# Performance work log

Hardware: AMD Instinct MI355X
Metric: run time of the kernel (lower is better)

## Reference

```python
import jax, jax.numpy as jnp
import numpy as np

B, S, D = 4, 2048, 512
H, DQK, DV = 6, 64, 64
PROJ = (DQK + DQK + DV) * H  # 1152
EPS = 1e-5


def setup_inputs() -> dict:
    key = jax.random.key(0)
    ks = jax.random.split(key, 5)
    sc = 0.05
    return {
        "x": jax.random.normal(ks[0], (B, S, D), jnp.float32),
        "Wp": jax.random.normal(ks[1], (PROJ, D), jnp.float32) * sc,
        "bp": jax.random.normal(ks[2], (PROJ,), jnp.float32) * sc,
        "Wo": jax.random.normal(ks[3], (D, H * DV), jnp.float32) * sc,
        "bo": jax.random.normal(ks[4], (D,), jnp.float32) * sc,
        "gamma": jnp.ones((D,), jnp.float32),
        "beta": jnp.zeros((D,), jnp.float32),
    }


def reference(x, Wp, bp, Wo, bo, gamma, beta):
    b, s, d = x.shape
    # 1x1 Conv1d projection == pointwise linear: [b,s,d] @ [d,proj] -> [b,s,proj]
    proj = jnp.einsum("bsd,pd->bsp", x, Wp) + bp
    q, k, v = proj[..., : H * DQK], proj[..., H * DQK : 2 * H * DQK], proj[..., 2 * H * DQK :]
    # split heads -> [b,h,s,depth]
    q = q.reshape(b, s, H, DQK).transpose(0, 2, 1, 3)
    k = k.reshape(b, s, H, DQK).transpose(0, 2, 1, 3)
    v = v.reshape(b, s, H, DV).transpose(0, 2, 1, 3)
    scores = jnp.einsum("bhqd,bhkd->bhqk", q, k) / jnp.sqrt(jnp.float32(DQK))
    attn = jax.nn.softmax(scores, axis=-1)  # softmax over kv axis
    out = jnp.einsum("bhqk,bhkd->bhqd", attn, v)
    # concat heads -> [b,s,h*dv]
    concat = out.transpose(0, 2, 1, 3).reshape(b, s, H * DV)
    y = jnp.einsum("bsf,df->bsd", concat, Wo) + bo
    z = x + y
    mu = jnp.mean(z, axis=-1, keepdims=True)
    var = jnp.mean(jnp.square(z - mu), axis=-1, keepdims=True)
    return (z - mu) / jnp.sqrt(var + EPS) * gamma + beta
```

## Files before the change

kernel.cpp:

```cpp
#include <hip/hip_runtime.h>

typedef __bf16 bf16;
typedef __bf16 bf16x8 __attribute__((ext_vector_type(8)));
typedef __bf16 bf16x4 __attribute__((ext_vector_type(4)));
typedef float  f32x4  __attribute__((ext_vector_type(4)));

#define BB 4
#define SS 2048
#define DD 512
#define HH 6
#define DH 64
#define PROJ 1152
#define FF 384
#define LDK 72

__device__ __forceinline__ bool probe_fp32(const unsigned* p) {
    return p[0] == 0x3F800000u;
}

__device__ __forceinline__ float fast_exp2(float x) {
#if __has_builtin(__builtin_amdgcn_exp2f)
    return __builtin_amdgcn_exp2f(x);
#else
    return __expf(x * 0.69314718f);
#endif
}

struct CvtSrcs { const void* s[7]; };

#define CB0 524288
#define CB1 598016
#define CB2 622592
#define CB3 622736
#define CB4 622800
#define CB5 622864
#define CB6 622928

__global__ __launch_bounds__(256) void cvt_all_kernel(
    CvtSrcs srcs, bf16* __restrict__ dst, const unsigned* __restrict__ probe)
{
    const int t = blockIdx.x * 256 + threadIdx.x;
    if (t >= CB6) return;
    int seg, base;
    if      (t < CB0) { seg = 0; base = 0;   }
    else if (t < CB1) { seg = 1; base = CB0; }
    else if (t < CB2) { seg = 2; base = CB1; }
    else if (t < CB3) { seg = 3; base = CB2; }
    else if (t < CB4) { seg = 4; base = CB3; }
    else if (t < CB5) { seg = 5; base = CB4; }
    else              { seg = 6; base = CB5; }
    const int li = (t - base) * 8;
    if (probe_fp32(probe)) {
        const float* s = (const float*)srcs.s[seg] + li;
        bf16x8 o;
#pragma unroll
        for (int j = 0; j < 8; ++j) o[j] = (bf16)s[j];
        *(bf16x8*)&dst[(size_t)t * 8] = o;
    } else {
        *(bf16x8*)&dst[(size_t)t * 8] =
            *(const bf16x8*)((const bf16*)srcs.s[seg] + li);
    }
}

template<int MERGE>
__global__ __launch_bounds__(256) void gemm_bt_kernel(
    const bf16* __restrict__ A, const float* __restrict__ lpart,
    const bf16* __restrict__ B, const bf16* __restrict__ bias,
    bf16* __restrict__ Cout, int M, int N, int K)
{
    __shared__ __attribute__((aligned(16))) bf16 sA[64 * LDK];
    __shared__ __attribute__((aligned(16))) bf16 sB[128 * LDK];

    const int tid  = threadIdx.x;
    const int lane = tid & 63;
    const int wave = tid >> 6;
    const int wn = wave * 32;
    const int l15 = lane & 15;
    const int quad = lane >> 4;
    const int bm = blockIdx.x * 64;
    const int bn = blockIdx.y * 128;
    const int KT = K / 64;

    int srowA[2], srowB[4];
    const int scol = (tid & 7) << 3;
#pragma unroll
    for (int j = 0; j < 2; ++j) srowA[j] = (j * 256 + tid) >> 3;
#pragma unroll
    for (int j = 0; j < 4; ++j) srowB[j] = (j * 256 + tid) >> 3;

    const bf16* pA[2]; const bf16* pB[4];
    const float* pl0[2];
#pragma unroll
    for (int j = 0; j < 2; ++j) {
        if (MERGE) {
            int row = bm + srowA[j];
            int b = row >> 11, q = row & (SS - 1);
            pA[j]  = A + ((size_t)(b * HH) * SS + q) * DH + scol;
            pl0[j] = lpart + (size_t)(b * HH) * SS + q;
        } else {
            pA[j] = A + (size_t)(bm + srowA[j]) * K + scol;
        }
    }
#pragma unroll
    for (int j = 0; j < 4; ++j)
        pB[j] = B + (size_t)(bn + srowB[j]) * K + scol;

    bf16x8 arb[2], a1b[2], brb[4];
    float l0[2], l1[2];

    auto loadAB = [&]() {
#pragma unroll
        for (int j = 0; j < 2; ++j) {
            arb[j] = *(const bf16x8*)pA[j];
            if (MERGE) {
                a1b[j] = *(const bf16x8*)(pA[j] + (size_t)BB * HH * SS * DH);
                l0[j] = pl0[j][0];
                l1[j] = pl0[j][(size_t)BB * HH * SS];
                pA[j]  += (size_t)SS * DH;
                pl0[j] += SS;
            } else {
                pA[j] += 64;
            }
        }
#pragma unroll
        for (int j = 0; j < 4; ++j) {
            brb[j] = *(const bf16x8*)pB[j];
            pB[j] += 64;
        }
    };

    loadAB();

    const f32x4 fzero = {0.f, 0.f, 0.f, 0.f};
    f32x4 acc[4][2];
#pragma unroll
    for (int mi = 0; mi < 4; ++mi)
#pragma unroll
        for (int ni = 0; ni < 2; ++ni) acc[mi][ni] = fzero;

    for (int kt = 0; kt < KT; ++kt) {
        __syncthreads();
#pragma unroll
        for (int j = 0; j < 2; ++j) {
            if (MERGE) {
                float inv = 1.f / (l0[j] + l1[j]);
                bf16x8 m;
#pragma unroll
                for (int e = 0; e < 8; ++e)
                    m[e] = (bf16)(((float)arb[j][e] + (float)a1b[j][e]) * inv);
                *(bf16x8*)&sA[srowA[j] * LDK + scol] = m;
            } else {
                *(bf16x8*)&sA[srowA[j] * LDK + scol] = arb[j];
            }
        }
#pragma unroll
        for (int j = 0; j < 4; ++j)
            *(bf16x8*)&sB[srowB[j] * LDK + scol] = brb[j];
        __syncthreads();
        if (kt + 1 < KT) loadAB();

#pragma unroll
        for (int kk = 0; kk < 2; ++kk) {
            bf16x8 af[4], bfr[2];
#pragma unroll
            for (int i = 0; i < 4; ++i)
                af[i] = *(const bf16x8*)&sA[(i * 16 + l15) * LDK + kk * 32 + quad * 8];
#pragma unroll
            for (int i = 0; i < 2; ++i)
                bfr[i] = *(const bf16x8*)&sB[(wn + i * 16 + l15) * LDK + kk * 32 + quad * 8];
#pragma unroll
            for (int mi = 0; mi < 4; ++mi)
#pragma unroll
                for (int ni = 0; ni < 2; ++ni)
                    acc[mi][ni] = __builtin_amdgcn_mfma_f32_16x16x32_bf16(
                        af[mi], bfr[ni], acc[mi][ni], 0, 0, 0);
        }
    }

#pragma unroll
    for (int mi = 0; mi < 4; ++mi) {
        int row = bm + mi * 16 + quad * 4;
#pragma unroll
        for (int ni = 0; ni < 2; ++ni) {
            int col = bn + wn + ni * 16 + l15;
            float bv = (float)bias[col];
#pragma unroll
            for (int r = 0; r < 4; ++r)
                Cout[(size_t)(row + r) * N + col] = (bf16)(acc[mi][ni][r] + bv);
        }
    }
}

__global__ __launch_bounds__(256) void vt_kernel(
    const bf16* __restrict__ proj, bf16* __restrict__ Vt)
{
    __shared__ __attribute__((aligned(16))) bf16 lt[64 * LDK];

    const int tid = threadIdx.x;
    const int s0 = blockIdx.x * 64;
    const int bh = blockIdx.y;
    const int b = bh / HH, h = bh % HH;

#pragma unroll
    for (int i = 0; i < 2; ++i) {
        int vid = i * 256 + tid;
        int sl = vid >> 3;
        int dc = (vid & 7) << 3;
        bf16x8 v = *(const bf16x8*)&proj[
            (size_t)(b * SS + s0 + sl) * PROJ + 2 * HH * DH + h * DH + dc];
#pragma unroll
        for (int j = 0; j < 8; ++j) {
            int d = dc + j;
            lt[d * LDK + (sl ^ (((d >> 3) & 3) * 8))] = v[j];
        }
    }
    __syncthreads();

#pragma unroll
    for (int i = 0; i < 2; ++i) {
        int vid = i * 256 + tid;
        int d = vid >> 3;
        int sc = (vid & 7) << 3;
        bf16x8 v = *(const bf16x8*)&lt[d * LDK + (sc ^ (((d >> 3) & 3) * 8))];
        *(bf16x8*)&Vt[(size_t)bh * DH * SS + (size_t)d * SS + s0 + sc] = v;
    }
}

__global__ __launch_bounds__(256) void attn_kernel(
    const bf16* __restrict__ proj, const bf16* __restrict__ Vt,
    bf16* __restrict__ Opart, float* __restrict__ lpart)
{
    __shared__ __attribute__((aligned(16))) bf16 sK [2][64 * 64];
    __shared__ __attribute__((aligned(16))) bf16 sVt[2][64 * 64];
    __shared__ __attribute__((aligned(16))) bf16 sP [4 * 32 * 64];

    const int tid  = threadIdx.x;
    const int lane = tid & 63;
    const int wave = tid >> 6;
    const int l15  = lane & 15;
    const int quad = lane >> 4;

    const int bh = blockIdx.y;
    const int b = bh / HH, h = bh % HH;
    const int q0 = blockIdx.x * 128;
    const int kz = blockIdx.z;
    const bf16* base = proj + (size_t)b * SS * PROJ;
    const bf16* vtb  = Vt + (size_t)bh * DH * SS;

    const int sr = tid >> 3;
    const int sc = (tid & 7) << 3;

    const float QS = 0.18033688f;
    bf16x8 qf[2][2];
#pragma unroll
    for (int g = 0; g < 2; ++g) {
        const int qrow = q0 + wave * 32 + g * 16 + l15;
#pragma unroll
        for (int ks = 0; ks < 2; ++ks) {
            qf[ks][g] = *(const bf16x8*)&base[
                (size_t)qrow * PROJ + h * DH + ks * 32 + quad * 8];
#pragma unroll
            for (int j = 0; j < 8; ++j)
                qf[ks][g][j] = (bf16)((float)qf[ks][g][j] * QS);
        }
    }

    const f32x4 fzero = {0.f, 0.f, 0.f, 0.f};
    f32x4 lacc[2] = {fzero, fzero};
    f32x4 oacc[2][4];
#pragma unroll
    for (int g = 0; g < 2; ++g)
#pragma unroll
        for (int fi = 0; fi < 4; ++fi) oacc[g][fi] = fzero;

    bf16* pw = &sP[wave * 32 * 64];

    const int kt0 = kz * (SS / 128);
    const int kt1 = kt0 + SS / 128;

    const bf16* pk[2]; const bf16* pv[2];
#pragma unroll
    for (int i = 0; i < 2; ++i) {
        int r = i * 32 + sr;
        pk[i] = &base[(size_t)(kt0 * 64 + r) * PROJ + HH * DH + h * DH + sc];
        pv[i] = &vtb[(size_t)r * SS + kt0 * 64 + sc];
    }

    bf16x8 kr[2], vr[2];
    auto loadKV = [&]() {
#pragma unroll
        for (int i = 0; i < 2; ++i) {
            kr[i] = *(const bf16x8*)pk[i];
            vr[i] = *(const bf16x8*)pv[i];
            pk[i] += (size_t)64 * PROJ;
            pv[i] += 64;
        }
    };
    auto stage = [&](int buf) {
#pragma unroll
        for (int i = 0; i < 2; ++i) {
            int r = i * 32 + sr;
            const int swc = sc ^ ((r & 7) << 3);
            *(bf16x8*)&sK [buf][r * 64 + swc] = kr[i];
            *(bf16x8*)&sVt[buf][r * 64 + swc] = vr[i];
        }
    };

    loadKV();
    stage(0);
    loadKV();

    for (int t = kt0; t < kt1; ++t) {
        const int cur = t & 1;
        __syncthreads();
        if (t + 1 < kt1) {
            stage(cur ^ 1);
            if (t + 2 < kt1) loadKV();
        }

        f32x4 st[2][4];
#pragma unroll
        for (int mi = 0; mi < 4; ++mi) {
            const int row = mi * 16 + l15;
            const int sw = (row & 7) << 3;
            bf16x8 af0 = *(const bf16x8*)&sK[cur][row * 64 + ((quad * 8) ^ sw)];
            bf16x8 af1 = *(const bf16x8*)&sK[cur][row * 64 + ((32 + quad * 8) ^ sw)];
            __builtin_amdgcn_s_setprio(1);
#pragma unroll
            for (int g = 0; g < 2; ++g) {
                st[g][mi] = __builtin_amdgcn_mfma_f32_16x16x32_bf16(
                    af0, qf[0][g], fzero, 0, 0, 0);
                st[g][mi] = __builtin_amdgcn_mfma_f32_16x16x32_bf16(
                    af1, qf[1][g], st[g][mi], 0, 0, 0);
            }
            __builtin_amdgcn_s_setprio(0);
        }

#pragma unroll
        for (int g = 0; g < 2; ++g)
#pragma unroll
            for (int mi = 0; mi < 4; ++mi) {
#pragma unroll
                for (int r = 0; r < 4; ++r)
                    st[g][mi][r] = fast_exp2(st[g][mi][r]);
                lacc[g] += st[g][mi];
            }

#pragma unroll
        for (int g = 0; g < 2; ++g) {
            const int r = g * 16 + l15;
            const int sw = (r & 7) << 3;
#pragma unroll
            for (int mi = 0; mi < 4; ++mi) {
                bf16x4 p4;
#pragma unroll
                for (int e = 0; e < 4; ++e) p4[e] = (bf16)st[g][mi][e];
                *(bf16x4*)&pw[r * 64 + ((mi * 16 + quad * 4) ^ sw)] = p4;
            }
        }

#pragma unroll
        for (int ks = 0; ks < 2; ++ks) {
            bf16x8 bfrag[2];
#pragma unroll
            for (int g = 0; g < 2; ++g) {
                const int r = g * 16 + l15;
                bfrag[g] = *(const bf16x8*)&pw[
                    r * 64 + ((ks * 32 + quad * 8) ^ ((r & 7) << 3))];
            }
#pragma unroll
            for (int fi = 0; fi < 4; ++fi) {
                const int row = fi * 16 + l15;
                bf16x8 af = *(const bf16x8*)&sVt[cur][
                    row * 64 + ((ks * 32 + quad * 8) ^ ((row & 7) << 3))];
                __builtin_amdgcn_s_setprio(1);
#pragma unroll
                for (int g = 0; g < 2; ++g)
                    oacc[g][fi] = __builtin_amdgcn_mfma_f32_16x16x32_bf16(
                        af, bfrag[g], oacc[g][fi], 0, 0, 0);
                __builtin_amdgcn_s_setprio(0);
            }
        }
    }

    float l_part[2];
#pragma unroll
    for (int g = 0; g < 2; ++g) {
        l_part[g] = lacc[g][0] + lacc[g][1] + lacc[g][2] + lacc[g][3];
        l_part[g] += __shfl_xor(l_part[g], 16);
        l_part[g] += __shfl_xor(l_part[g], 32);
    }

    const size_t zoff = (size_t)(kz * BB * HH + bh) * SS;
#pragma unroll
    for (int g = 0; g < 2; ++g) {
        const int qg = q0 + wave * 32 + g * 16 + l15;
        bf16* orow = Opart + (zoff + qg) * DH;
#pragma unroll
        for (int fi = 0; fi < 4; ++fi) {
            bf16x4 o4;
#pragma unroll
            for (int r = 0; r < 4; ++r) o4[r] = (bf16)oacc[g][fi][r];
            *(bf16x4*)&orow[fi * 16 + quad * 4] = o4;
        }
    }
    if (lane < 16) {
#pragma unroll
        for (int g = 0; g < 2; ++g)
            lpart[zoff + q0 + wave * 32 + g * 16 + lane] = l_part[g];
    }
}

__global__ __launch_bounds__(256) void ln_kernel(
    const bf16* __restrict__ x, const bf16* __restrict__ y,
    const bf16* __restrict__ gamma, const bf16* __restrict__ beta,
    void* __restrict__ out, const unsigned* __restrict__ probe)
{
    const bool f32 = probe_fp32(probe);
    const int lane = threadIdx.x & 63;
    const int wave = threadIdx.x >> 6;
    const int row = blockIdx.x * 4 + wave;
    const size_t off = (size_t)row * DD + lane * 8;

    bf16x8 xv = *(const bf16x8*)&x[off];
    bf16x8 yv = *(const bf16x8*)&y[off];
    float z[8];
    float s = 0.f;
#pragma unroll
    for (int j = 0; j < 8; ++j) { z[j] = (float)xv[j] + (float)yv[j]; s += z[j]; }
#pragma unroll
    for (int m = 1; m < 64; m <<= 1) s += __shfl_xor(s, m);
    float mu = s * (1.f / DD);
    float s2 = 0.f;
#pragma unroll
    for (int j = 0; j < 8; ++j) { float d = z[j] - mu; s2 += d * d; }
#pragma unroll
    for (int m = 1; m < 64; m <<= 1) s2 += __shfl_xor(s2, m);
    float rs = rsqrtf(s2 * (1.f / DD) + 1e-5f);

    bf16x8 gm = *(const bf16x8*)&gamma[lane * 8];
    bf16x8 be = *(const bf16x8*)&beta[lane * 8];
    if (f32) {
        f32x4 o0, o1;
#pragma unroll
        for (int j = 0; j < 4; ++j) {
            o0[j] = (z[j]     - mu) * rs * (float)gm[j]     + (float)be[j];
            o1[j] = (z[j + 4] - mu) * rs * (float)gm[j + 4] + (float)be[j + 4];
        }
        *(f32x4*)&((float*)out)[off]     = o0;
        *(f32x4*)&((float*)out)[off + 4] = o1;
    } else {
        bf16x8 o;
#pragma unroll
        for (int j = 0; j < 8; ++j)
            o[j] = (bf16)((z[j] - mu) * rs * (float)gm[j] + (float)be[j]);
        *(bf16x8*)&((bf16*)out)[off] = o;
    }
}

extern "C" void kernel_launch(void* const* d_in, const int* in_sizes, int n_in,
                              void* d_out, int out_size, void* d_ws, size_t ws_size,
                              hipStream_t stream)
{
    const unsigned* probe = (const unsigned*)d_in[5];

    char* ws = (char*)d_ws;
    size_t o = 0;
    bf16* xb   = (bf16*)(ws + o); o += (size_t)BB * SS * DD * 2;
    bf16* Wpb  = (bf16*)(ws + o); o += (size_t)PROJ * DD * 2;
    bf16* Wob  = (bf16*)(ws + o); o += (size_t)DD * FF * 2;
    bf16* bpb  = (bf16*)(ws + o); o += PROJ * 2;
    bf16* bob  = (bf16*)(ws + o); o += DD * 2;
    bf16* gb   = (bf16*)(ws + o); o += DD * 2;
    bf16* bb   = (bf16*)(ws + o); o += DD * 2;
    bf16* proj   = (bf16*)(ws + o); o += (size_t)BB * SS * PROJ * 2;
    bf16* vtbuf  = (bf16*)(ws + o); o += (size_t)BB * HH * DH * SS * 2;
    bf16* Opart  = (bf16*)(ws + o); o += (size_t)2 * BB * HH * SS * DH * 2;
    float* lpart = (float*)(ws + o); o += (size_t)2 * BB * HH * SS * 4;
    bf16* ybuf = proj;

    CvtSrcs srcs;
    srcs.s[0] = d_in[0]; srcs.s[1] = d_in[1]; srcs.s[2] = d_in[3];
    srcs.s[3] = d_in[2]; srcs.s[4] = d_in[4]; srcs.s[5] = d_in[5];
    srcs.s[6] = d_in[6];
    cvt_all_kernel<<<(CB6 + 255) / 256, 256, 0, stream>>>(srcs, xb, probe);

    gemm_bt_kernel<0><<<dim3((BB * SS) / 64, PROJ / 128), 256, 0, stream>>>(
        xb, nullptr, Wpb, bpb, proj, BB * SS, PROJ, DD);
    vt_kernel<<<dim3(SS / 64, BB * HH), 256, 0, stream>>>(proj, vtbuf);
    attn_kernel<<<dim3(SS / 128, BB * HH, 2), 256, 0, stream>>>(
        proj, vtbuf, Opart, lpart);
    gemm_bt_kernel<1><<<dim3((BB * SS) / 64, DD / 128), 256, 0, stream>>>(
        Opart, lpart, Wob, bob, ybuf, BB * SS, DD, FF);
    ln_kernel<<<dim3((BB * SS) / 4), 256, 0, stream>>>(
        xb, ybuf, gb, bb, d_out, probe);
}
```

Before: 155.7 us.

## Load K/V MFMA fragments directly from global memory, dropping shared staging

The attention kernel no longer stages K and V^T tiles through double-buffered shared memory with block-wide barriers. Each wave now loads its own MFMA fragments for K and V straight from global memory into registers, prefetching the next tile between the QK and PV phases. This removes the __syncthreads and LDS traffic, but all four waves redundantly fetch the same K/V data (4x more global/L2 traffic), uses more registers, and performs strided uncoalesced row loads.

```diff
diff --git a/kernel.cpp b/kernel.cpp
--- a/kernel.cpp
+++ b/kernel.cpp
@@ -230,9 +230,7 @@
     const bf16* __restrict__ proj, const bf16* __restrict__ Vt,
     bf16* __restrict__ Opart, float* __restrict__ lpart)
 {
-    __shared__ __attribute__((aligned(16))) bf16 sK [2][64 * 64];
-    __shared__ __attribute__((aligned(16))) bf16 sVt[2][64 * 64];
-    __shared__ __attribute__((aligned(16))) bf16 sP [4 * 32 * 64];
+    __shared__ __attribute__((aligned(16))) bf16 sP[4 * 32 * 64];
 
     const int tid  = threadIdx.x;
     const int lane = tid & 63;
@@ -245,10 +243,8 @@
     const int q0 = blockIdx.x * 128;
     const int kz = blockIdx.z;
     const bf16* base = proj + (size_t)b * SS * PROJ;
-    const bf16* vtb  = Vt + (size_t)bh * DH * SS;
-
-    const int sr = tid >> 3;
-    const int sc = (tid & 7) << 3;
+    const bf16* kbase = base + HH * DH + h * DH + quad * 8;
+    const bf16* vtb = Vt + (size_t)bh * DH * SS;
 
     const float QS = 0.18033688f;
     bf16x8 qf[2][2];
@@ -278,109 +274,78 @@
     const int kt0 = kz * (SS / 128);
     const int kt1 = kt0 + SS / 128;
 
-    const bf16* pk[2]; const bf16* pv[2];
-#pragma unroll
-    for (int i = 0; i < 2; ++i) {
-        int r = i * 32 + sr;
-        pk[i] = &base[(size_t)(kt0 * 64 + r) * PROJ + HH * DH + h * DH + sc];
-        pv[i] = &vtb[(size_t)r * SS + kt0 * 64 + sc];
-    }
-
-    bf16x8 kr[2], vr[2];
-    auto loadKV = [&]() {
-#pragma unroll
-        for (int i = 0; i < 2; ++i) {
-            kr[i] = *(const bf16x8*)pk[i];
-            vr[i] = *(const bf16x8*)pv[i];
-            pk[i] += (size_t)64 * PROJ;
-            pv[i] += 64;
-        }
+    bf16x8 kfr[2][4], vfr[2][4];
+    auto loadK = [&](int kt) {
+        const bf16* p = kbase + (size_t)(kt * 64 + l15) * PROJ;
+#pragma unroll
+        for (int mi = 0; mi < 4; ++mi)
+#pragma unroll
+            for (int ks = 0; ks < 2; ++ks)
+                kfr[ks][mi] = *(const bf16x8*)(p + (size_t)(mi * 16) * PROJ + ks * 32);
     };
-    auto stage = [&](int buf) {
-#pragma unroll
-        for (int i = 0; i < 2; ++i) {
-            int r = i * 32 + sr;
-            const int swc = sc ^ ((r & 7) << 3);
-            *(bf16x8*)&sK [buf][r * 64 + swc] = kr[i];
-            *(bf16x8*)&sVt[buf][r * 64 + swc] = vr[i];
-        }
+    auto loadV = [&](int kt) {
+        const bf16* p = vtb + (size_t)l15 * SS + kt * 64 + quad * 8;
+#pragma unroll
+        for (int fi = 0; fi < 4; ++fi)
+#pragma unroll
+            for (int ks = 0; ks < 2; ++ks)
+                vfr[ks][fi] = *(const bf16x8*)(p + (size_t)(fi * 16) * SS + ks * 32);
     };
 
-    loadKV();
-    stage(0);
-    loadKV();
+    loadK(kt0);
+    loadV(kt0);
 
     for (int t = kt0; t < kt1; ++t) {
-        const int cur = t & 1;
-        __syncthreads();
-        if (t + 1 < kt1) {
-            stage(cur ^ 1);
-            if (t + 2 < kt1) loadKV();
-        }
-
-        f32x4 st[2][4];
 #pragma unroll
         for (int mi = 0; mi < 4; ++mi) {
-            const int row = mi * 16 + l15;
-            const int sw = (row & 7) << 3;
-            bf16x8 af0 = *(const bf16x8*)&sK[cur][row * 64 + ((quad * 8) ^ sw)];
-            bf16x8 af1 = *(const bf16x8*)&sK[cur][row * 64 + ((32 + quad * 8) ^ sw)];
+            f32x4 st[2];
             __builtin_amdgcn_s_setprio(1);
 #pragma unroll
             for (int g = 0; g < 2; ++g) {
-                st[g][mi] = __builtin_amdgcn_mfma_f32_16x16x32_bf16(
-                    af0, qf[0][g], fzero, 0, 0, 0);
-                st[g][mi] = __builtin_amdgcn_mfma_f32_16x16x32_bf16(
-                    af1, qf[1][g], st[g][mi], 0, 0, 0);
+                st[g] = __builtin_amdgcn_mfma_f32_16x16x32_bf16(
+                    kfr[0][mi], qf[0][g], fzero, 0, 0, 0);
+                st[g] = __builtin_amdgcn_mfma_f32_16x16x32_bf16(
+                    kfr[1][mi], qf[1][g], st[g], 0, 0, 0);
             }
             __builtin_amdgcn_s_setprio(0);
-        }
-
-#pragma unroll
-        for (int g = 0; g < 2; ++g)
-#pragma unroll
-            for (int mi = 0; mi < 4; ++mi) {
+#pragma unroll
+            for (int g = 0; g < 2; ++g) {
 #pragma unroll
                 for (int r = 0; r < 4; ++r)
-                    st[g][mi][r] = fast_exp2(st[g][mi][r]);
-                lacc[g] += st[g][mi];
-            }
-
-#pragma unroll
-        for (int g = 0; g < 2; ++g) {
-            const int r = g * 16 + l15;
-            const int sw = (r & 7) << 3;
-#pragma unroll
-            for (int mi = 0; mi < 4; ++mi) {
+                    st[g][r] = fast_exp2(st[g][r]);
+                lacc[g] += st[g];
+                const int rr = g * 16 + l15;
+                const int sw = (rr & 7) << 3;
                 bf16x4 p4;
 #pragma unroll
-                for (int e = 0; e < 4; ++e) p4[e] = (bf16)st[g][mi][e];
-                *(bf16x4*)&pw[r * 64 + ((mi * 16 + quad * 4) ^ sw)] = p4;
-            }
-        }
+                for (int e = 0; e < 4; ++e) p4[e] = (bf16)st[g][e];
+                *(bf16x4*)&pw[rr * 64 + ((mi * 16 + quad * 4) ^ sw)] = p4;
+            }
+        }
+
+        if (t + 1 < kt1) loadK(t + 1);
 
 #pragma unroll
         for (int ks = 0; ks < 2; ++ks) {
             bf16x8 bfrag[2];
 #pragma unroll
             for (int g = 0; g < 2; ++g) {
-                const int r = g * 16 + l15;
+                const int rr = g * 16 + l15;
                 bfrag[g] = *(const bf16x8*)&pw[
-                    r * 64 + ((ks * 32 + quad * 8) ^ ((r & 7) << 3))];
+                    rr * 64 + ((ks * 32 + quad * 8) ^ ((rr & 7) << 3))];
             }
 #pragma unroll
             for (int fi = 0; fi < 4; ++fi) {
-                const int row = fi * 16 + l15;
-                bf16x8 af = *(const bf16x8*)&sVt[cur][
-                    row * 64 + ((ks * 32 + quad * 8) ^ ((row & 7) << 3))];
                 __builtin_amdgcn_s_setprio(1);
 #pragma unroll
                 for (int g = 0; g < 2; ++g)
                     oacc[g][fi] = __builtin_amdgcn_mfma_f32_16x16x32_bf16(
-                        af, bfrag[g], oacc[g][fi], 0, 0, 0);
+                        vfr[ks][fi], bfrag[g], oacc[g][fi], 0, 0, 0);
                 __builtin_amdgcn_s_setprio(0);
             }
         }
+
+        if (t + 1 < kt1) loadV(t + 1);
     }
 
     float l_part[2];
```

After: 209.6 us. 34.6% more time.
